# Performance work log

Measured on AMD Instinct MI355X. Metric: run time of the kernel, lower is better.

The kernel has to match this reference:

```python
import jax, jax.numpy as jnp
import numpy as np
import math

B, S, D, H = 2, 2048, 768, 12
HD = D // H


def setup_inputs() -> dict:
    key = jax.random.key(0)
    ks = jax.random.split(key, 9)
    scale = 1.0 / math.sqrt(D)
    x = jax.random.normal(ks[0], (B, S, D), dtype=jnp.float32)
    # causal mask: True where attention is allowed (query i attends to key j<=i)
    mask = jnp.tril(jnp.ones((S, S), dtype=bool))[None, None]  # [1,1,S,S]
    wq = jax.random.normal(ks[1], (D, D), dtype=jnp.float32) * scale
    bq = jnp.zeros((D,), dtype=jnp.float32)
    wk = jax.random.normal(ks[2], (D, D), dtype=jnp.float32) * scale
    bk = jnp.zeros((D,), dtype=jnp.float32)
    wv = jax.random.normal(ks[3], (D, D), dtype=jnp.float32) * scale
    bv = jnp.zeros((D,), dtype=jnp.float32)
    wo = jax.random.normal(ks[4], (D, D), dtype=jnp.float32) * scale
    bo = jnp.zeros((D,), dtype=jnp.float32)
    return {"x": x, "mask": mask, "wq": wq, "bq": bq, "wk": wk, "bk": bk,
            "wv": wv, "bv": bv, "wo": wo, "bo": bo}


def reference(x, mask, wq, bq, wk, bk, wv, bv, wo, bo):
    b, s, d = x.shape
    # projections (flax Linear: y = x @ kernel + bias)
    q = (x @ wq + bq).reshape(b, s, H, HD).transpose(0, 2, 1, 3)  # [b,h,s,hd]
    k = (x @ wk + bk).reshape(b, s, H, HD).transpose(0, 2, 1, 3)
    v = (x @ wv + bv).reshape(b, s, H, HD).transpose(0, 2, 1, 3)
    scores = jnp.einsum('bhqd,bhkd->bhqk', q, k) / math.sqrt(HD)  # [b,h,s,s]
    scores = jnp.where(mask, scores, -jnp.inf)
    attn = jax.nn.softmax(scores, axis=-1)
    out = jnp.einsum('bhqk,bhkd->bhqd', attn, v)  # [b,h,s,hd]
    out = out.transpose(0, 2, 1, 3).reshape(b, s, d)
    return out @ wo + bo
```

## Files before the change

kernel.cpp:

```cpp
#include <hip/hip_runtime.h>
#include <math.h>

#define BATCH 2
#define SEQ   2048
#define DMODEL 768
#define NHEAD 12
#define HDIM  64

typedef unsigned short u16;
typedef __attribute__((ext_vector_type(8))) short bf16x8;
typedef __attribute__((ext_vector_type(4))) float f32x4;
typedef __attribute__((ext_vector_type(8))) unsigned short us8;
typedef __attribute__((ext_vector_type(4))) unsigned short us4;

__device__ __forceinline__ u16 f2bf(float f) {
    union { float f; unsigned u; } v; v.f = f;
    unsigned u = v.u;
    u += 0x7fff + ((u >> 16) & 1);
    return (u16)(u >> 16);
}

__device__ __forceinline__ u16 f2bf_trunc(float f) {
    union { float f; unsigned u; } v; v.f = f;
    return (u16)(v.u >> 16);
}

__device__ __forceinline__ void g2l16(const void* g, void* l) {
    __builtin_amdgcn_global_load_lds(
        (const __attribute__((address_space(1))) unsigned int*)g,
        (__attribute__((address_space(3))) unsigned int*)(unsigned int)(unsigned long long)(uintptr_t)l,
        16, 0, 0);
}

__device__ __forceinline__ void stage_rows(const u16* g, u16* lds, int nrows,
                                           int tid) {
    const int row = tid >> 2, col = (tid & 3) * 8;
    g2l16(g + (size_t)row * DMODEL + col, lds + tid * 8);
    if (nrows == 128) {
        g2l16(g + (size_t)(row + 64) * DMODEL + col, lds + 2048 + tid * 8);
    } else if (nrows == 96) {
        if (tid < 128)
            g2l16(g + (size_t)(row + 64) * DMODEL + col, lds + 2048 + tid * 8);
    }
}

__global__ __launch_bounds__(256) void prep(const float* __restrict__ x,
                                            const float* __restrict__ w0,
                                            const float* __restrict__ w1,
                                            const float* __restrict__ w2,
                                            const float* __restrict__ w3,
                                            u16* __restrict__ xb,
                                            u16* __restrict__ Wt_all) {
    __shared__ float t[32][33];
    const int bid = blockIdx.x;
    if (bid < 3072) {
        int i = bid * 256 + threadIdx.x;
        float4 v = ((const float4*)x)[i];
        us4 o;
        o.x = f2bf(v.x); o.y = f2bf(v.y); o.z = f2bf(v.z); o.w = f2bf(v.w);
        *(us4*)&xb[(size_t)i * 4] = o;
    } else {
        const int wid = bid - 3072;
        const int z  = wid / 576;
        const int rr = wid % 576;
        const int by = rr / 24, bx = rr % 24;
        const float* W = z == 0 ? w0 : z == 1 ? w1 : z == 2 ? w2 : w3;
        u16* Wt = Wt_all + (size_t)z * DMODEL * DMODEL;

        int tx = threadIdx.x & 31, ty = threadIdx.x >> 5;
        int xg = bx * 32 + tx;
        #pragma unroll
        for (int j = 0; j < 32; j += 8)
            t[ty + j][tx] = W[(size_t)(by * 32 + ty + j) * DMODEL + xg];
        __syncthreads();
        int x2 = by * 32 + tx;
        #pragma unroll
        for (int j = 0; j < 32; j += 8)
            Wt[(size_t)(bx * 32 + ty + j) * DMODEL + x2] = f2bf(t[tx][ty + j]);
    }
}

__global__ __launch_bounds__(256) void gemm_qkv(
    const u16* __restrict__ xb, const u16* __restrict__ WtQK,
    const u16* __restrict__ WtV,
    const float* __restrict__ bq, const float* __restrict__ bk,
    const float* __restrict__ bv,
    u16* __restrict__ QK, u16* __restrict__ Vt) {

    __shared__ __align__(16) u16 As[128 * 32];
    __shared__ __align__(16) u16 Bs[128 * 32];

    const int tid  = threadIdx.x;
    const int lane = tid & 63;
    const int w    = tid >> 6;
    const int quad = lane >> 4, l16 = lane & 15;
    const int wm   = w >> 1, wn = w & 1;
    const int b    = blockIdx.x;

    if (b < 512) {
        const int m0 = (b >> 4) * 128;
        const int n0 = (b & 15) * 96;
        f32x4 acc[4][3] = {};
        for (int k0 = 0; k0 < DMODEL; k0 += 32) {
            stage_rows(xb   + (size_t)m0 * DMODEL + k0, As, 128, tid);
            stage_rows(WtQK + (size_t)n0 * DMODEL + k0, Bs,  96, tid);
            __syncthreads();
            bf16x8 af[4], bfr[3];
            #pragma unroll
            for (int i = 0; i < 4; ++i)
                af[i] = *(const bf16x8*)&As[(wm * 64 + i * 16 + l16) * 32 + quad * 8];
            #pragma unroll
            for (int j = 0; j < 3; ++j)
                bfr[j] = *(const bf16x8*)&Bs[(wn * 48 + j * 16 + l16) * 32 + quad * 8];
            #pragma unroll
            for (int i = 0; i < 4; ++i)
                #pragma unroll
                for (int j = 0; j < 3; ++j)
                    acc[i][j] = __builtin_amdgcn_mfma_f32_16x16x32_bf16(af[i], bfr[j], acc[i][j], 0, 0, 0);
            __syncthreads();
        }
        const size_t n_elem = (size_t)BATCH * SEQ * DMODEL;
        #pragma unroll
        for (int j = 0; j < 3; ++j) {
            const int n     = n0 + wn * 48 + j * 16 + l16;
            const int which = n / 768;
            const int nn    = n - which * 768;
            const float bias  = (which == 0 ? bq : bk)[nn];
            const float scale = (which == 0) ? 0.125f : 1.0f;
            const int h = nn >> 6, hd = nn & 63;
            u16* outw = QK + (size_t)which * n_elem;
            #pragma unroll
            for (int i = 0; i < 4; ++i) {
                const int mbase = m0 + wm * 64 + i * 16 + quad * 4;
                #pragma unroll
                for (int r = 0; r < 4; ++r) {
                    const int m  = mbase + r;
                    const int b_ = m >> 11, s_ = m & 2047;
                    outw[(size_t)((b_ * NHEAD + h) * SEQ + s_) * HDIM + hd] =
                        f2bf((acc[i][j][r] + bias) * scale);
                }
            }
        }
    } else {
        const int vj = b - 512;
        const int m0 = (vj & 7) * 96;
        const int n0 = (vj >> 3) * 128;
        f32x4 acc[3][4] = {};
        for (int k0 = 0; k0 < DMODEL; k0 += 32) {
            stage_rows(WtV + (size_t)m0 * DMODEL + k0, As,  96, tid);
            stage_rows(xb  + (size_t)n0 * DMODEL + k0, Bs, 128, tid);
            __syncthreads();
            bf16x8 af[3], bfr[4];
            #pragma unroll
            for (int i = 0; i < 3; ++i)
                af[i] = *(const bf16x8*)&As[(wm * 48 + i * 16 + l16) * 32 + quad * 8];
            #pragma unroll
            for (int j = 0; j < 4; ++j)
                bfr[j] = *(const bf16x8*)&Bs[(wn * 64 + j * 16 + l16) * 32 + quad * 8];
            #pragma unroll
            for (int i = 0; i < 3; ++i)
                #pragma unroll
                for (int j = 0; j < 4; ++j)
                    acc[i][j] = __builtin_amdgcn_mfma_f32_16x16x32_bf16(af[i], bfr[j], acc[i][j], 0, 0, 0);
            __syncthreads();
        }
        #pragma unroll
        for (int i = 0; i < 3; ++i) {
            const int rbase = m0 + wm * 48 + i * 16 + quad * 4;
            #pragma unroll
            for (int r = 0; r < 4; ++r) {
                const int row_g = rbase + r;
                const float bias = bv[row_g];
                const int h = row_g >> 6, hd = row_g & 63;
                #pragma unroll
                for (int j = 0; j < 4; ++j) {
                    const int col_g = n0 + wn * 64 + j * 16 + l16;
                    const int b_ = col_g >> 11, s_ = col_g & 2047;
                    Vt[(size_t)((b_ * NHEAD + h) * HDIM + hd) * SEQ + s_] =
                        f2bf(acc[i][j][r] + bias);
                }
            }
        }
    }
}

__global__ __launch_bounds__(256) void gemm_out(
    const u16* __restrict__ Ag, const u16* __restrict__ Bt,
    const float* __restrict__ bo, float* __restrict__ out) {

    __shared__ __align__(16) u16 As[64 * 32];
    __shared__ __align__(16) u16 Bs[64 * 32];

    const int tid  = threadIdx.x;
    const int lane = tid & 63;
    const int w    = tid >> 6;
    const int quad = lane >> 4, l16 = lane & 15;
    const int wm   = w >> 1, wn = w & 1;
    const int m0 = blockIdx.x * 64, n0 = blockIdx.y * 64;

    const int rowA = tid >> 2;
    const int kch  = (tid & 3) * 8;

    f32x4 acc[2][2] = {};

    for (int k0 = 0; k0 < DMODEL; k0 += 32) {
        g2l16(Ag + (size_t)(m0 + rowA) * DMODEL + k0 + kch, As + tid * 8);
        g2l16(Bt + (size_t)(n0 + rowA) * DMODEL + k0 + kch, Bs + tid * 8);
        __syncthreads();

        bf16x8 af[2], bfr[2];
        #pragma unroll
        for (int i = 0; i < 2; ++i)
            af[i] = *(const bf16x8*)&As[(wm * 32 + i * 16 + l16) * 32 + quad * 8];
        #pragma unroll
        for (int j = 0; j < 2; ++j)
            bfr[j] = *(const bf16x8*)&Bs[(wn * 32 + j * 16 + l16) * 32 + quad * 8];
        #pragma unroll
        for (int i = 0; i < 2; ++i)
            #pragma unroll
            for (int j = 0; j < 2; ++j)
                acc[i][j] = __builtin_amdgcn_mfma_f32_16x16x32_bf16(af[i], bfr[j], acc[i][j], 0, 0, 0);
        __syncthreads();
    }

    #pragma unroll
    for (int i = 0; i < 2; ++i) {
        const int mbase = m0 + wm * 32 + i * 16 + quad * 4;
        #pragma unroll
        for (int r = 0; r < 4; ++r) {
            const int m = mbase + r;
            #pragma unroll
            for (int j = 0; j < 2; ++j) {
                const int n = n0 + wn * 32 + j * 16 + l16;
                out[(size_t)m * DMODEL + n] = acc[i][j][r] + bo[n];
            }
        }
    }
}

__global__ __launch_bounds__(256) void flash_attn_mfma(
    const u16* __restrict__ Q, const u16* __restrict__ K,
    const u16* __restrict__ Vt, u16* __restrict__ A) {

    __shared__ __align__(16) u16 Kl[64 * 72];
    __shared__ __align__(16) u16 Vl[64 * 72];
    __shared__ __align__(16) u16 Pl[4][16 * 72];

    const int tid  = threadIdx.x;
    const int lane = tid & 63;
    const int w    = tid >> 6;
    const int quad = lane >> 4;
    const int l16  = lane & 15;

    const int bh = blockIdx.x;
    const int p  = blockIdx.y;
    const int uq = (w < 2) ? p : 63 - p;
    const int wrow0 = uq * 32 + (w & 1) * 16;
    const int wlast = wrow0 + 15;

    const size_t base = (size_t)bh * SEQ * HDIM;
    const u16* Qg = Q + base;
    const u16* Kg = K + base;
    const u16* Vg = Vt + base;

    bf16x8 qf0 = *(const bf16x8*)&Qg[(size_t)(wrow0 + l16) * 64 + quad * 8];
    bf16x8 qf1 = *(const bf16x8*)&Qg[(size_t)(wrow0 + l16) * 64 + quad * 8 + 32];

    f32x4 o[4] = {};
    float l_acc[4] = {0.f, 0.f, 0.f, 0.f};

    const int qrow = wrow0 + quad * 4;
    const int uB = 63 - p;
    const int tc = (32 * uB + 31) / 64 + 1;

    const int pwbase = 2 * quad + (l16 >> 3);
    const int prd0   = (quad + 2 * (l16 >> 2)) & 7;
    u16* Pw = Pl[w];
    const u16* pr0 = &Pw[l16 * 72 + prd0 * 8];
    const u16* pr1 = &Pw[l16 * 72 + (prd0 ^ 4) * 8];

    for (int t2 = 0; t2 < tc; ++t2) {
        const int j0 = t2 * 64;
        __syncthreads();

        #pragma unroll
        for (int r = 0; r < 2; ++r) {
            int e = tid + r * 256;
            int row = e >> 3, col = (e & 7) * 8;
            *(us8*)&Kl[row * 72 + col] = *(const us8*)&Kg[(size_t)(j0 + row) * 64 + col];
        }
        #pragma unroll
        for (int r = 0; r < 2; ++r) {
            int e = tid + r * 256;
            int d = e >> 3, kc = (e & 7) * 8;
            *(us8*)&Vl[d * 72 + kc] = *(const us8*)&Vg[(size_t)d * SEQ + j0 + kc];
        }
        __syncthreads();

        if (j0 > wlast) continue;

        f32x4 s[4];
        #pragma unroll
        for (int c4 = 0; c4 < 4; ++c4) {
            bf16x8 kf0 = *(const bf16x8*)&Kl[(c4 * 16 + l16) * 72 + quad * 8];
            bf16x8 kf1 = *(const bf16x8*)&Kl[(c4 * 16 + l16) * 72 + quad * 8 + 32];
            f32x4 a2 = {};
            a2 = __builtin_amdgcn_mfma_f32_16x16x32_bf16(qf0, kf0, a2, 0, 0, 0);
            a2 = __builtin_amdgcn_mfma_f32_16x16x32_bf16(qf1, kf1, a2, 0, 0, 0);
            s[c4] = a2;
        }

        if (j0 + 63 > wrow0) {
            #pragma unroll
            for (int c4 = 0; c4 < 4; ++c4) {
                int jg = j0 + c4 * 16 + l16;
                #pragma unroll
                for (int r = 0; r < 4; ++r)
                    if (jg > qrow + r) s[c4][r] = -INFINITY;
            }
        }

        #pragma unroll
        for (int c4 = 0; c4 < 4; ++c4)
            #pragma unroll
            for (int r = 0; r < 4; ++r)
                s[c4][r] = __expf(s[c4][r]);
        #pragma unroll
        for (int r = 0; r < 4; ++r)
            l_acc[r] += (s[0][r] + s[1][r]) + (s[2][r] + s[3][r]);

        #pragma unroll
        for (int c4 = 0; c4 < 4; ++c4) {
            const int pc = ((2 * c4 + pwbase) & 7) * 8 + (l16 & 7);
            #pragma unroll
            for (int r = 0; r < 4; ++r)
                Pw[(quad * 4 + r) * 72 + pc] = f2bf_trunc(s[c4][r]);
        }
        bf16x8 pf0 = *(const bf16x8*)pr0;
        bf16x8 pf1 = *(const bf16x8*)pr1;

        #pragma unroll
        for (int c2 = 0; c2 < 4; ++c2) {
            bf16x8 vf0 = *(const bf16x8*)&Vl[(c2 * 16 + l16) * 72 + quad * 8];
            bf16x8 vf1 = *(const bf16x8*)&Vl[(c2 * 16 + l16) * 72 + quad * 8 + 32];
            o[c2] = __builtin_amdgcn_mfma_f32_16x16x32_bf16(pf0, vf0, o[c2], 0, 0, 0);
            o[c2] = __builtin_amdgcn_mfma_f32_16x16x32_bf16(pf1, vf1, o[c2], 0, 0, 0);
        }
    }

    #pragma unroll
    for (int off = 1; off < 16; off <<= 1)
        #pragma unroll
        for (int r = 0; r < 4; ++r)
            l_acc[r] += __shfl_xor(l_acc[r], off);

    const int b = bh / NHEAD, h = bh % NHEAD;
    #pragma unroll
    for (int r = 0; r < 4; ++r) {
        float inv = 1.0f / l_acc[r];
        int sg = qrow + r;
        u16* dst = A + ((size_t)(b * SEQ + sg)) * DMODEL + h * HDIM;
        #pragma unroll
        for (int c2 = 0; c2 < 4; ++c2)
            dst[c2 * 16 + l16] = f2bf(o[c2][r] * inv);
    }
}

extern "C" void kernel_launch(void* const* d_in, const int* in_sizes, int n_in,
                              void* d_out, int out_size, void* d_ws, size_t ws_size,
                              hipStream_t stream) {
    const float* x  = (const float*)d_in[0];
    const float* wq = (const float*)d_in[2];
    const float* bq = (const float*)d_in[3];
    const float* wk = (const float*)d_in[4];
    const float* bk = (const float*)d_in[5];
    const float* wv = (const float*)d_in[6];
    const float* bv = (const float*)d_in[7];
    const float* wo = (const float*)d_in[8];
    const float* bo = (const float*)d_in[9];
    float* out = (float*)d_out;

    const size_t n_elem = (size_t)BATCH * SEQ * DMODEL;
    const size_t w_elem = (size_t)DMODEL * DMODEL;

    u16* xb     = (u16*)d_ws;
    u16* Wt_all = xb + n_elem;
    u16* Qw     = Wt_all + 4 * w_elem;
    u16* Vtw    = Qw + 2 * n_elem;
    u16* Aw     = Vtw + n_elem;

    dim3 blk(256);

    prep<<<dim3(3072 + 2304), blk, 0, stream>>>(x, wq, wk, wv, wo, xb, Wt_all);

    gemm_qkv<<<dim3(768), blk, 0, stream>>>(xb, Wt_all, Wt_all + 2 * w_elem,
                                            bq, bk, bv, Qw, Vtw);

    flash_attn_mfma<<<dim3(24, 32), blk, 0, stream>>>(Qw, Qw + n_elem, Vtw, Aw);

    gemm_out<<<dim3(64, 12), blk, 0, stream>>>(Aw, Wt_all + 3 * w_elem, bo, out);
}
```

Measured before the change: 169.3 us.

## Split flash-attention KV loop across wave pairs and merge partials in LDS

Doubles the attention block to 512 threads. Each pair of waves shares the same 16 query rows and takes alternate 64-key tiles, so each wave handles half the key tiles. The partial O and row sums are merged through LDS, which is unioned with the K/V tiles. The aim is to shorten the serial per-wave KV loop and raise parallelism, at the cost of an extra LDS reduction, more threads per block, and half the waves sitting idle at each tile barrier.

```diff
diff --git a/kernel.cpp b/kernel.cpp
--- a/kernel.cpp
+++ b/kernel.cpp
@@ -238,24 +238,28 @@
     }
 }
 
-__global__ __launch_bounds__(256) void flash_attn_mfma(
+__global__ __launch_bounds__(512) void flash_attn_mfma(
     const u16* __restrict__ Q, const u16* __restrict__ K,
     const u16* __restrict__ Vt, u16* __restrict__ A) {
 
-    __shared__ __align__(16) u16 Kl[64 * 72];
-    __shared__ __align__(16) u16 Vl[64 * 72];
-    __shared__ __align__(16) u16 Pl[4][16 * 72];
+    __shared__ __align__(16) union {
+        struct { u16 Kl[64 * 72]; u16 Vl[64 * 72]; } kv;
+        struct { float O[4][16][66]; float L[4][16]; } ep;
+    } sm;
+    __shared__ __align__(16) u16 Pl[8][16 * 72];
 
     const int tid  = threadIdx.x;
     const int lane = tid & 63;
     const int w    = tid >> 6;
+    const int s    = w >> 1;
+    const int e    = w & 1;
     const int quad = lane >> 4;
     const int l16  = lane & 15;
 
     const int bh = blockIdx.x;
     const int p  = blockIdx.y;
-    const int uq = (w < 2) ? p : 63 - p;
-    const int wrow0 = uq * 32 + (w & 1) * 16;
+    const int uq = (s < 2) ? p : 63 - p;
+    const int wrow0 = uq * 32 + (s & 1) * 16;
     const int wlast = wrow0 + 15;
 
     const size_t base = (size_t)bh * SEQ * HDIM;
@@ -270,8 +274,7 @@
     float l_acc[4] = {0.f, 0.f, 0.f, 0.f};
 
     const int qrow = wrow0 + quad * 4;
-    const int uB = 63 - p;
-    const int tc = (32 * uB + 31) / 64 + 1;
+    const int tc = ((63 - p) >> 1) + 1;
 
     const int pwbase = 2 * quad + (l16 >> 3);
     const int prd0   = (quad + 2 * (l16 >> 2)) & 7;
@@ -283,31 +286,30 @@
         const int j0 = t2 * 64;
         __syncthreads();
 
-        #pragma unroll
-        for (int r = 0; r < 2; ++r) {
-            int e = tid + r * 256;
-            int row = e >> 3, col = (e & 7) * 8;
-            *(us8*)&Kl[row * 72 + col] = *(const us8*)&Kg[(size_t)(j0 + row) * 64 + col];
-        }
-        #pragma unroll
-        for (int r = 0; r < 2; ++r) {
-            int e = tid + r * 256;
-            int d = e >> 3, kc = (e & 7) * 8;
-            *(us8*)&Vl[d * 72 + kc] = *(const us8*)&Vg[(size_t)d * SEQ + j0 + kc];
+        {
+            int row = tid >> 3, col = (tid & 7) * 8;
+            *(us8*)&sm.kv.Kl[row * 72 + col] =
+                *(const us8*)&Kg[(size_t)(j0 + row) * 64 + col];
+        }
+        {
+            int d = tid >> 3, kc = (tid & 7) * 8;
+            *(us8*)&sm.kv.Vl[d * 72 + kc] =
+                *(const us8*)&Vg[(size_t)d * SEQ + j0 + kc];
         }
         __syncthreads();
 
+        if ((t2 & 1) != e) continue;
         if (j0 > wlast) continue;
 
-        f32x4 s[4];
+        f32x4 sc[4];
         #pragma unroll
         for (int c4 = 0; c4 < 4; ++c4) {
-            bf16x8 kf0 = *(const bf16x8*)&Kl[(c4 * 16 + l16) * 72 + quad * 8];
-            bf16x8 kf1 = *(const bf16x8*)&Kl[(c4 * 16 + l16) * 72 + quad * 8 + 32];
+            bf16x8 kf0 = *(const bf16x8*)&sm.kv.Kl[(c4 * 16 + l16) * 72 + quad * 8];
+            bf16x8 kf1 = *(const bf16x8*)&sm.kv.Kl[(c4 * 16 + l16) * 72 + quad * 8 + 32];
             f32x4 a2 = {};
             a2 = __builtin_amdgcn_mfma_f32_16x16x32_bf16(qf0, kf0, a2, 0, 0, 0);
             a2 = __builtin_amdgcn_mfma_f32_16x16x32_bf16(qf1, kf1, a2, 0, 0, 0);
-            s[c4] = a2;
+            sc[c4] = a2;
         }
 
         if (j0 + 63 > wrow0) {
@@ -316,7 +318,7 @@
                 int jg = j0 + c4 * 16 + l16;
                 #pragma unroll
                 for (int r = 0; r < 4; ++r)
-                    if (jg > qrow + r) s[c4][r] = -INFINITY;
+                    if (jg > qrow + r) sc[c4][r] = -INFINITY;
             }
         }
 
@@ -324,25 +326,25 @@
         for (int c4 = 0; c4 < 4; ++c4)
             #pragma unroll
             for (int r = 0; r < 4; ++r)
-                s[c4][r] = __expf(s[c4][r]);
+                sc[c4][r] = __expf(sc[c4][r]);
         #pragma unroll
         for (int r = 0; r < 4; ++r)
-            l_acc[r] += (s[0][r] + s[1][r]) + (s[2][r] + s[3][r]);
+            l_acc[r] += (sc[0][r] + sc[1][r]) + (sc[2][r] + sc[3][r]);
 
         #pragma unroll
         for (int c4 = 0; c4 < 4; ++c4) {
             const int pc = ((2 * c4 + pwbase) & 7) * 8 + (l16 & 7);
             #pragma unroll
             for (int r = 0; r < 4; ++r)
-                Pw[(quad * 4 + r) * 72 + pc] = f2bf_trunc(s[c4][r]);
+                Pw[(quad * 4 + r) * 72 + pc] = f2bf_trunc(sc[c4][r]);
         }
         bf16x8 pf0 = *(const bf16x8*)pr0;
         bf16x8 pf1 = *(const bf16x8*)pr1;
 
         #pragma unroll
         for (int c2 = 0; c2 < 4; ++c2) {
-            bf16x8 vf0 = *(const bf16x8*)&Vl[(c2 * 16 + l16) * 72 + quad * 8];
-            bf16x8 vf1 = *(const bf16x8*)&Vl[(c2 * 16 + l16) * 72 + quad * 8 + 32];
+            bf16x8 vf0 = *(const bf16x8*)&sm.kv.Vl[(c2 * 16 + l16) * 72 + quad * 8];
+            bf16x8 vf1 = *(const bf16x8*)&sm.kv.Vl[(c2 * 16 + l16) * 72 + quad * 8 + 32];
             o[c2] = __builtin_amdgcn_mfma_f32_16x16x32_bf16(pf0, vf0, o[c2], 0, 0, 0);
             o[c2] = __builtin_amdgcn_mfma_f32_16x16x32_bf16(pf1, vf1, o[c2], 0, 0, 0);
         }
@@ -354,15 +356,31 @@
         for (int r = 0; r < 4; ++r)
             l_acc[r] += __shfl_xor(l_acc[r], off);
 
-    const int b = bh / NHEAD, h = bh % NHEAD;
-    #pragma unroll
-    for (int r = 0; r < 4; ++r) {
-        float inv = 1.0f / l_acc[r];
-        int sg = qrow + r;
-        u16* dst = A + ((size_t)(b * SEQ + sg)) * DMODEL + h * HDIM;
-        #pragma unroll
-        for (int c2 = 0; c2 < 4; ++c2)
-            dst[c2 * 16 + l16] = f2bf(o[c2][r] * inv);
+    __syncthreads();
+    if (e == 0) {
+        #pragma unroll
+        for (int r = 0; r < 4; ++r) {
+            #pragma unroll
+            for (int c2 = 0; c2 < 4; ++c2)
+                sm.ep.O[s][quad * 4 + r][c2 * 16 + l16] = o[c2][r];
+            if (l16 == 0) sm.ep.L[s][quad * 4 + r] = l_acc[r];
+        }
+    }
+    __syncthreads();
+    if (e == 1) {
+        const int b = bh / NHEAD, h = bh % NHEAD;
+        #pragma unroll
+        for (int r = 0; r < 4; ++r) {
+            float lt = l_acc[r] + sm.ep.L[s][quad * 4 + r];
+            float inv = 1.0f / lt;
+            int sg = qrow + r;
+            u16* dst = A + ((size_t)(b * SEQ + sg)) * DMODEL + h * HDIM;
+            #pragma unroll
+            for (int c2 = 0; c2 < 4; ++c2) {
+                float ov = o[c2][r] + sm.ep.O[s][quad * 4 + r][c2 * 16 + l16];
+                dst[c2 * 16 + l16] = f2bf(ov * inv);
+            }
+        }
     }
 }
 
@@ -396,7 +414,8 @@
     gemm_qkv<<<dim3(768), blk, 0, stream>>>(xb, Wt_all, Wt_all + 2 * w_elem,
                                             bq, bk, bv, Qw, Vtw);
 
-    flash_attn_mfma<<<dim3(24, 32), blk, 0, stream>>>(Qw, Qw + n_elem, Vtw, Aw);
+    flash_attn_mfma<<<dim3(24, 32), dim3(512), 0, stream>>>(Qw, Qw + n_elem,
+                                                            Vtw, Aw);
 
     gemm_out<<<dim3(64, 12), blk, 0, stream>>>(Aw, Wt_all + 3 * w_elem, bo, out);
 }
```

After: 169.2 us. Within noise of the previous version (-0.0%).
